# Kernel tuning notes

Measured on AMD Instinct MI355X. Metric: run time of the kernel, lower is better.

The kernel has to match this reference:

```python
import jax, jax.numpy as jnp
import numpy as np

T, NTOK, D = 8, 32768, 128
N_ENTIRE, COMP_LEN, COMP_DIM = 65536, 8, 64


def _layer_norm(v, w, b, eps=1e-5):
    m = v.mean(-1, keepdims=True)
    c = v - m
    var = (c * c).mean(-1, keepdims=True)
    return c * jax.lax.rsqrt(var + eps) * w + b


def setup_inputs() -> dict:
    key = jax.random.key(0)
    ks = jax.random.split(key, 8)
    x = jax.random.normal(ks[0], (T, NTOK, D), jnp.float32)
    padded_node_mask = jnp.ones((T, NTOK), dtype=bool)  # all tokens are nodes
    # unique per-timestamp scatter indices into the 'entire node' axis
    node_idx = jax.vmap(lambda k: jax.random.permutation(k, N_ENTIRE)[:NTOK])(
        jax.random.split(ks[1], T)).astype(jnp.int32)
    s = 0.02
    return dict(
        x=x,
        ln1_w=jnp.ones((D,), jnp.float32), ln1_b=jnp.zeros((D,), jnp.float32),
        w1=jax.random.normal(ks[2], (D, 2 * COMP_DIM), jnp.float32) * s,
        b1=jnp.zeros((2 * COMP_DIM,), jnp.float32),
        w2=jax.random.normal(ks[3], (2 * COMP_DIM, COMP_DIM), jnp.float32) * s,
        b2=jnp.zeros((COMP_DIM,), jnp.float32),
        lnf_w=jnp.ones((COMP_LEN * COMP_DIM,), jnp.float32),
        lnf_b=jnp.zeros((COMP_LEN * COMP_DIM,), jnp.float32),
        padded_node_mask=padded_node_mask,
        node_idx=node_idx,
        n_entire=N_ENTIRE,
    )


def reference(x, ln1_w, ln1_b, w1, b1, w2, b2, lnf_w, lnf_b,
              padded_node_mask, node_idx, n_entire):
    t, ntok, d = x.shape
    # encode_layer_norm over all tokens
    xn = _layer_norm(x, ln1_w, ln1_b)
    # nodes = xn[padded_node_mask].reshape(t, ntok, d); mask is all-True here
    nodes = jnp.where(padded_node_mask[..., None], xn, 0.0)
    # scga._to_entire: scatter nodes into [t, n_entire, d] (zeros elsewhere)
    tenodes = jnp.zeros((t, n_entire, d), x.dtype)
    tenodes = tenodes.at[jnp.arange(t)[:, None], node_idx].set(nodes)
    # eval mode: np.array_split(arange(n_entire), comp_len) = equal contiguous groups
    g = n_entire // COMP_LEN
    xg = tenodes.reshape(t, COMP_LEN, g, d)  # [t, L, g, d]
    # per-group MLP (Linear->GELU->(Dropout=id)->Linear) then mean over group
    h = jax.nn.gelu(jnp.einsum('tlgd,de->tlge', xg, w1) + b1, approximate=False)
    c = jnp.einsum('tlge,ec->tlgc', h, w2) + b2
    comp = c.mean(axis=2)  # [t, L, comp_dim]
    compressed = _layer_norm(comp.reshape(t, 1, COMP_LEN * COMP_DIM), lnf_w, lnf_b)
    # orthogonality loss over the L compressed components (exact torch pair loop)
    f = comp.transpose(1, 0, 2).reshape(COMP_LEN, -1)  # [L, t*comp_dim]
    fn = f / jnp.linalg.norm(f, axis=-1, keepdims=True)
    dots = []
    for i in range(COMP_LEN - 1):
        for j in range(1, COMP_LEN):
            dots.append(jnp.sum(fn[i] * fn[j]) / jnp.sum(fn[i] + fn[j]))
    ortho_loss = jnp.mean(jnp.stack(dots) ** 2)
    return compressed, ortho_loss
```

## Files before the change

### kernel.cpp

```cpp
#include <hip/hip_runtime.h>
#include <math.h>

#define TT 8
#define NTOK 32768
#define DD 128
#define LCOMP 8
#define GSZ 8192
#define CDIM 64
#define EDIM 128
#define NPART 32

#define TOKB 64
#define TILES 4
#define NBLK (TT*NTOK/(TOKB*TILES))

#define O_CZERO 0
#define O_W2BT  256
#define O_W1BT  (256 + EDIM*CDIM*2)
#define O_CSUMP (O_W1BT + DD*EDIM*2)

typedef __attribute__((ext_vector_type(8))) short bf16x8;
typedef __attribute__((ext_vector_type(4))) float f32x4;

__device__ __forceinline__ ushort f2bf(float f) {
    union { float f; uint u; } c; c.f = f;
    uint u = c.u;
    return (ushort)((u + 0x7FFFu + ((u >> 16) & 1u)) >> 16);
}

__device__ __forceinline__ float gelu_f(float a) {
    float x = a * 0.70710678118654752f;
    float ax = fabsf(x);
    float t = 1.0f / (1.0f + 0.3275911f * ax);
    float p = t * (0.254829592f + t * (-0.284496736f + t * (1.421413741f +
              t * (-1.453152027f + t * 1.061405429f))));
    float e = __expf(-x * x);
    float er = copysignf(1.0f - p * e, x);
    return 0.5f * a * (1.0f + er);
}

__global__ void prep_kernel(const float* __restrict__ w1, const float* __restrict__ b1,
                            const float* __restrict__ w2,
                            ushort* __restrict__ w1bt, ushort* __restrict__ w2bt,
                            float* __restrict__ czero, float* __restrict__ csum_p) {
    int gid = blockIdx.x * 256 + threadIdx.x;
    if (gid < DD * EDIM) {
        int j = gid >> 7, d = gid & 127;
        int slot = (d >> 3) ^ (j & 7);
        w1bt[j * 128 + slot * 8 + (d & 7)] = f2bf(w1[d * EDIM + j]);
    }
    if (gid < EDIM * CDIM) {
        int k = gid >> 7, jj = gid & 127;
        w2bt[k * 128 + jj] = f2bf(w2[jj * CDIM + k]);
    }
    if (gid < CDIM) {
        float a2 = 0.f;
        for (int dd = 0; dd < EDIM; ++dd)
            a2 += gelu_f(b1[dd]) * w2[dd * CDIM + gid];
        czero[gid] = a2;
    }
#pragma unroll
    for (int i = 0; i < 8; ++i)
        csum_p[gid + i * 16384] = 0.f;
}

__global__ __launch_bounds__(256, 2)
void main_kernel(const float* __restrict__ x,
                 const float* __restrict__ ln1w, const float* __restrict__ ln1b,
                 const float* __restrict__ b1g,
                 const ushort* __restrict__ w1bt, const ushort* __restrict__ w2bt,
                 const float* __restrict__ czero,
                 const int* __restrict__ node_idx,
                 float* __restrict__ csum_p) {
    __shared__ ushort s_xn[TOKB * DD];
    __shared__ ushort s_h[TOKB * DD];
    __shared__ float  s_acc[LCOMP * CDIM];

    const int tid = threadIdx.x;
    const int w   = tid >> 6;
    const int ln  = tid & 63;
    const int cs  = ln >> 4;
    const int row = w * 16 + (ln & 15);
    const int bid = blockIdx.x;
    const size_t base0 = (size_t)bid * (TOKB * TILES);

    s_acc[tid] = 0.f; s_acc[tid + 256] = 0.f;

    const float b1v0 = b1g[w * 32 + (ln & 15)];
    const float b1v1 = b1g[w * 32 + 16 + (ln & 15)];
    float czv[4];
#pragma unroll
    for (int kt = 0; kt < 4; ++kt) czv[kt] = czero[kt * 16 + (ln & 15)];

    float v[32];
    {
        const float* xp = x + (base0 + row) * DD + cs * 32;
#pragma unroll
        for (int sx = 0; sx < 8; ++sx) {
            float4 f = *(const float4*)(xp + sx * 4);
            v[sx*4+0]=f.x; v[sx*4+1]=f.y; v[sx*4+2]=f.z; v[sx*4+3]=f.w;
        }
    }

    for (int tile = 0; tile < TILES; ++tile) {
        {
            float s = 0.f, q = 0.f;
#pragma unroll
            for (int i2 = 0; i2 < 32; ++i2) { s += v[i2]; q += v[i2]*v[i2]; }
            s += __shfl_xor(s, 16, 64); q += __shfl_xor(q, 16, 64);
            s += __shfl_xor(s, 32, 64); q += __shfl_xor(q, 32, 64);
            float m   = s * (1.f/128.f);
            float var = q * (1.f/128.f) - m*m;
            float rs  = rsqrtf(var + 1e-5f);
#pragma unroll
            for (int sx = 0; sx < 8; ++sx) {
                float4 w4 = *(const float4*)(ln1w + cs*32 + sx*4);
                float4 b4 = *(const float4*)(ln1b + cs*32 + sx*4);
                v[sx*4+0] = (v[sx*4+0]-m)*rs*w4.x + b4.x;
                v[sx*4+1] = (v[sx*4+1]-m)*rs*w4.y + b4.y;
                v[sx*4+2] = (v[sx*4+2]-m)*rs*w4.z + b4.z;
                v[sx*4+3] = (v[sx*4+3]-m)*rs*w4.w + b4.w;
            }
        }
#pragma unroll
        for (int u = 0; u < 4; ++u) {
            uint4 pk;
            pk.x = f2bf(v[u*8+0]) | ((uint)f2bf(v[u*8+1]) << 16);
            pk.y = f2bf(v[u*8+2]) | ((uint)f2bf(v[u*8+3]) << 16);
            pk.z = f2bf(v[u*8+4]) | ((uint)f2bf(v[u*8+5]) << 16);
            pk.w = f2bf(v[u*8+6]) | ((uint)f2bf(v[u*8+7]) << 16);
            int slot = (cs * 4 + u) ^ (row & 7);
            *(uint4*)((char*)s_xn + row * 256 + slot * 16) = pk;
        }
        __syncthreads();

        if (tile + 1 < TILES) {
            const float* xp = x + (base0 + (tile + 1) * TOKB + row) * DD + cs * 32;
#pragma unroll
            for (int sx = 0; sx < 8; ++sx) {
                float4 f = *(const float4*)(xp + sx * 4);
                v[sx*4+0]=f.x; v[sx*4+1]=f.y; v[sx*4+2]=f.z; v[sx*4+3]=f.w;
            }
        }

        bf16x8 b1f[2][4];
#pragma unroll
        for (int jt = 0; jt < 2; ++jt)
#pragma unroll
            for (int ks = 0; ks < 4; ++ks) {
                int jrow = w * 32 + jt * 16 + (ln & 15);
                int slot = (ks * 4 + cs) ^ (jrow & 7);
                b1f[jt][ks] = *(const bf16x8*)((const char*)w1bt + jrow * 256 + slot * 16);
            }
#pragma unroll
        for (int tt = 0; tt < 4; ++tt) {
            bf16x8 a4[4];
            int ar = tt * 16 + (ln & 15);
#pragma unroll
            for (int ks = 0; ks < 4; ++ks) {
                int slot = (ks * 4 + cs) ^ (ar & 7);
                a4[ks] = *(const bf16x8*)((const char*)s_xn + ar * 256 + slot * 16);
            }
            f32x4 ac0 = {0.f,0.f,0.f,0.f}, ac1 = {0.f,0.f,0.f,0.f};
#pragma unroll
            for (int ks = 0; ks < 4; ++ks) {
                ac0 = __builtin_amdgcn_mfma_f32_16x16x32_bf16(a4[ks], b1f[0][ks], ac0, 0, 0, 0);
                ac1 = __builtin_amdgcn_mfma_f32_16x16x32_bf16(a4[ks], b1f[1][ks], ac1, 0, 0, 0);
            }
            int hrb = tt * 16 + cs * 4;
            int j0  = w * 32 + (ln & 15);
            int j1  = j0 + 16;
#pragma unroll
            for (int r = 0; r < 4; ++r) {
                float h0 = gelu_f(ac0[r] + b1v0);
                float h1 = gelu_f(ac1[r] + b1v1);
                int hrow = hrb + r;
                int sl0 = (j0 >> 3) ^ (hrow & 7);
                int sl1 = (j1 >> 3) ^ (hrow & 7);
                *(ushort*)((char*)s_h + hrow*256 + sl0*16 + (j0 & 7)*2) = f2bf(h0);
                *(ushort*)((char*)s_h + hrow*256 + sl1*16 + (j1 & 7)*2) = f2bf(h1);
            }
        }
        __syncthreads();

        {
            bf16x8 a4[4];
            int ar = w * 16 + (ln & 15);
#pragma unroll
            for (int ks = 0; ks < 4; ++ks) {
                int slot = (ks * 4 + cs) ^ (ar & 7);
                a4[ks] = *(const bf16x8*)((const char*)s_h + ar * 256 + slot * 16);
            }
            int tok0 = w * 16 + cs * 4;
            int4 li = *(const int4*)(node_idx + base0 + (size_t)tile * TOKB + tok0);
            int l0 = li.x >> 13, l1 = li.y >> 13, l2 = li.z >> 13, l3 = li.w >> 13;
#pragma unroll
            for (int kt = 0; kt < 4; ++kt) {
                bf16x8 bfr[4];
                int krow = kt * 16 + (ln & 15);
#pragma unroll
                for (int ks = 0; ks < 4; ++ks)
                    bfr[ks] = *(const bf16x8*)(w2bt + krow * EDIM + ks * 32 + cs * 8);
                f32x4 acc = {0.f,0.f,0.f,0.f};
#pragma unroll
                for (int ks = 0; ks < 4; ++ks)
                    acc = __builtin_amdgcn_mfma_f32_16x16x32_bf16(a4[ks], bfr[ks], acc, 0, 0, 0);
                int k = kt * 16 + (ln & 15);
                float czk = czv[kt];
                atomicAdd(&s_acc[l0 * CDIM + k], acc[0] - czk);
                atomicAdd(&s_acc[l1 * CDIM + k], acc[1] - czk);
                atomicAdd(&s_acc[l2 * CDIM + k], acc[2] - czk);
                atomicAdd(&s_acc[l3 * CDIM + k], acc[3] - czk);
            }
        }
        __syncthreads();
    }

    {
        int t8 = (bid >> 7) * LCOMP;
        int p  = bid & (NPART - 1);
#pragma unroll
        for (int i2 = 0; i2 < 2; ++i2) {
            int idx = tid + i2 * 256;
            int l = idx >> 6, k = idx & 63;
            atomicAdd(&csum_p[(p * 64 + t8 + l) * 64 + k], s_acc[idx]);
        }
    }
}

__global__ void fin_kernel(const float* __restrict__ csum_p, const float* __restrict__ czero,
                           const float* __restrict__ b2,
                           const float* __restrict__ lnfw, const float* __restrict__ lnfb,
                           float* __restrict__ out) {
    __shared__ float comp[TT * LCOMP * CDIM];
    __shared__ float norm_s[LCOMP], sum_s[LCOMP], red[8];
    int tid = threadIdx.x;

    for (int idx = tid; idx < TT * LCOMP * CDIM; idx += 512) {
        int bin = idx >> 6, k = idx & 63;
        float s = 0.f;
        for (int p = 0; p < NPART; ++p) s += csum_p[(p * 64 + bin) * 64 + k];
        comp[idx] = s * (1.f / GSZ) + czero[k] + b2[k];
    }
    __syncthreads();

    int wave = tid >> 6, lane = tid & 63;

    {
        int t = wave;
        float s = 0.f, q = 0.f;
        for (int e = lane; e < 512; e += 64) {
            float v = comp[t * 512 + e];
            s += v; q += v * v;
        }
#pragma unroll
        for (int off = 32; off > 0; off >>= 1) {
            s += __shfl_xor(s, off, 64);
            q += __shfl_xor(q, off, 64);
        }
        float m = s * (1.f / 512.f);
        float var = q * (1.f / 512.f) - m * m;
        float rs = rsqrtf(var + 1e-5f);
        for (int e = lane; e < 512; e += 64) {
            float v = comp[t * 512 + e];
            out[t * 512 + e] = (v - m) * rs * lnfw[e] + lnfb[e];
        }
    }

    {
        int l = wave;
        float s2 = 0.f, s1 = 0.f;
        for (int qd = lane; qd < 512; qd += 64) {
            int t = qd >> 6, k = qd & 63;
            float v = comp[t * 512 + l * 64 + k];
            s2 += v * v; s1 += v;
        }
#pragma unroll
        for (int off = 32; off > 0; off >>= 1) {
            s2 += __shfl_xor(s2, off, 64);
            s1 += __shfl_xor(s1, off, 64);
        }
        if (lane == 0) { norm_s[l] = sqrtf(s2); sum_s[l] = s1; }
    }
    __syncthreads();

    float loss_part = 0.f;
    for (int p = wave; p < 49; p += 8) {
        int i = p / 7, j = 1 + p % 7;
        float d = 0.f;
        for (int qd = lane; qd < 512; qd += 64) {
            int t = qd >> 6, k = qd & 63;
            d += comp[t * 512 + i * 64 + k] * comp[t * 512 + j * 64 + k];
        }
#pragma unroll
        for (int off = 32; off > 0; off >>= 1) d += __shfl_xor(d, off, 64);
        float ni = norm_s[i], nj = norm_s[j];
        float dot = (d / (ni * nj)) / (sum_s[i] / ni + sum_s[j] / nj);
        loss_part += dot * dot;
    }
    if (lane == 0) red[wave] = loss_part;
    __syncthreads();
    if (tid == 0) {
        float tot = 0.f;
        for (int w2_ = 0; w2_ < 8; ++w2_) tot += red[w2_];
        out[4096] = tot * (1.f / 49.f);
    }
}

extern "C" void kernel_launch(void* const* d_in, const int* in_sizes, int n_in,
                              void* d_out, int out_size, void* d_ws, size_t ws_size,
                              hipStream_t stream) {
    const float* x    = (const float*)d_in[0];
    const float* ln1w = (const float*)d_in[1];
    const float* ln1b = (const float*)d_in[2];
    const float* w1   = (const float*)d_in[3];
    const float* b1   = (const float*)d_in[4];
    const float* w2   = (const float*)d_in[5];
    const float* b2   = (const float*)d_in[6];
    const float* lnfw = (const float*)d_in[7];
    const float* lnfb = (const float*)d_in[8];
    const int* node_idx = (const int*)d_in[10];
    float* out = (float*)d_out;

    char* wsb = (char*)d_ws;
    float*  czero  = (float*)(wsb + O_CZERO);
    ushort* w2bt   = (ushort*)(wsb + O_W2BT);
    ushort* w1bt   = (ushort*)(wsb + O_W1BT);
    float*  csum_p = (float*)(wsb + O_CSUMP);

    prep_kernel<<<64, 256, 0, stream>>>(w1, b1, w2, w1bt, w2bt, czero, csum_p);
    main_kernel<<<NBLK, 256, 0, stream>>>(x, ln1w, ln1b, b1, w1bt, w2bt, czero,
                                          node_idx, csum_p);
    fin_kernel<<<1, 512, 0, stream>>>(csum_p, czero, b2, lnfw, lnfb, out);
}
```

Baseline: 365.0 us.

## Keep MLP weights in registers and run per-wave token batches without block syncs

Each wave now loads all W1 and W2 bf16 fragments into registers once and handles its own 16-token batches. LayerNorm output goes straight into MFMA operand registers, and the GELU result makes only a short round trip through per-wave shared memory. Block-level __syncthreads between tiles and shared staging of xn are gone, and the transposed formulation lets bias and czero seed the accumulators. Blocks are larger and there are fewer global partial sums. The cost is much higher register pressure, which may reduce occupancy, plus per-token shared atomics with possible bank contention.

After: 391.0 us. 7.1% more time.

```diff
diff --git a/kernel.cpp b/kernel.cpp
--- a/kernel.cpp
+++ b/kernel.cpp
@@ -8,11 +8,13 @@
 #define GSZ 8192
 #define CDIM 64
 #define EDIM 128
-#define NPART 32
-
-#define TOKB 64
-#define TILES 4
-#define NBLK (TT*NTOK/(TOKB*TILES))
+#define NPART 8
+
+#define BATCH 16
+#define BPW 8
+#define WAVES 4
+#define TOKBLK (WAVES*BPW*BATCH)
+#define NBLK (TT*NTOK/TOKBLK)
 
 #define O_CZERO 0
 #define O_W2BT  256
@@ -46,8 +48,7 @@
     int gid = blockIdx.x * 256 + threadIdx.x;
     if (gid < DD * EDIM) {
         int j = gid >> 7, d = gid & 127;
-        int slot = (d >> 3) ^ (j & 7);
-        w1bt[j * 128 + slot * 8 + (d & 7)] = f2bf(w1[d * EDIM + j]);
+        w1bt[j * 128 + d] = f2bf(w1[d * EDIM + j]);
     }
     if (gid < EDIM * CDIM) {
         int k = gid >> 7, jj = gid & 127;
@@ -60,7 +61,7 @@
         czero[gid] = a2;
     }
 #pragma unroll
-    for (int i = 0; i < 8; ++i)
+    for (int i = 0; i < 2; ++i)
         csum_p[gid + i * 16384] = 0.f;
 }
 
@@ -72,158 +73,153 @@
                  const float* __restrict__ czero,
                  const int* __restrict__ node_idx,
                  float* __restrict__ csum_p) {
-    __shared__ ushort s_xn[TOKB * DD];
-    __shared__ ushort s_h[TOKB * DD];
-    __shared__ float  s_acc[LCOMP * CDIM];
+    __shared__ ushort s_h[WAVES * 2048];
+    __shared__ float  s_acc[LCOMP * 65];
 
     const int tid = threadIdx.x;
     const int w   = tid >> 6;
     const int ln  = tid & 63;
     const int cs  = ln >> 4;
-    const int row = w * 16 + (ln & 15);
+    const int tk  = ln & 15;
     const int bid = blockIdx.x;
-    const size_t base0 = (size_t)bid * (TOKB * TILES);
-
-    s_acc[tid] = 0.f; s_acc[tid + 256] = 0.f;
-
-    const float b1v0 = b1g[w * 32 + (ln & 15)];
-    const float b1v1 = b1g[w * 32 + 16 + (ln & 15)];
-    float czv[4];
-#pragma unroll
-    for (int kt = 0; kt < 4; ++kt) czv[kt] = czero[kt * 16 + (ln & 15)];
+
+    for (int idx = tid; idx < LCOMP * 65; idx += 256) s_acc[idx] = 0.f;
+
+    bf16x8 w1f[8][4];
+#pragma unroll
+    for (int jt = 0; jt < 8; ++jt)
+#pragma unroll
+        for (int ks = 0; ks < 4; ++ks)
+            w1f[jt][ks] = *(const bf16x8*)(w1bt + (jt*16 + tk)*128 + ks*32 + cs*8);
+    bf16x8 w2f[4][4];
+#pragma unroll
+    for (int kt = 0; kt < 4; ++kt)
+#pragma unroll
+        for (int ks = 0; ks < 4; ++ks)
+            w2f[kt][ks] = *(const bf16x8*)(w2bt + (kt*16 + tk)*128 + ks*32 + cs*8);
+    f32x4 b1v[8];
+#pragma unroll
+    for (int jt = 0; jt < 8; ++jt)
+        b1v[jt] = *(const f32x4*)(b1g + jt*16 + cs*4);
+    f32x4 czv[4];
+#pragma unroll
+    for (int kt = 0; kt < 4; ++kt)
+        czv[kt] = -*(const f32x4*)(czero + kt*16 + cs*4);
+
+    __syncthreads();
+
+    const size_t wbase = (size_t)bid * TOKBLK + w * (BPW * BATCH);
+    char* hbase = (char*)s_h + w * 4096;
 
     float v[32];
     {
-        const float* xp = x + (base0 + row) * DD + cs * 32;
-#pragma unroll
-        for (int sx = 0; sx < 8; ++sx) {
-            float4 f = *(const float4*)(xp + sx * 4);
-            v[sx*4+0]=f.x; v[sx*4+1]=f.y; v[sx*4+2]=f.z; v[sx*4+3]=f.w;
-        }
-    }
-
-    for (int tile = 0; tile < TILES; ++tile) {
-        {
-            float s = 0.f, q = 0.f;
-#pragma unroll
-            for (int i2 = 0; i2 < 32; ++i2) { s += v[i2]; q += v[i2]*v[i2]; }
-            s += __shfl_xor(s, 16, 64); q += __shfl_xor(q, 16, 64);
-            s += __shfl_xor(s, 32, 64); q += __shfl_xor(q, 32, 64);
-            float m   = s * (1.f/128.f);
-            float var = q * (1.f/128.f) - m*m;
-            float rs  = rsqrtf(var + 1e-5f);
-#pragma unroll
-            for (int sx = 0; sx < 8; ++sx) {
-                float4 w4 = *(const float4*)(ln1w + cs*32 + sx*4);
-                float4 b4 = *(const float4*)(ln1b + cs*32 + sx*4);
-                v[sx*4+0] = (v[sx*4+0]-m)*rs*w4.x + b4.x;
-                v[sx*4+1] = (v[sx*4+1]-m)*rs*w4.y + b4.y;
-                v[sx*4+2] = (v[sx*4+2]-m)*rs*w4.z + b4.z;
-                v[sx*4+3] = (v[sx*4+3]-m)*rs*w4.w + b4.w;
+        const float* xp = x + (wbase + tk) * (size_t)DD;
+#pragma unroll
+        for (int m = 0; m < 4; ++m) {
+            *(float4*)(v + m*8)     = *(const float4*)(xp + m*32 + cs*8);
+            *(float4*)(v + m*8 + 4) = *(const float4*)(xp + m*32 + cs*8 + 4);
+        }
+    }
+
+    for (int b = 0; b < BPW; ++b) {
+        const size_t tb = wbase + (size_t)b * BATCH;
+        const int lg = node_idx[tb + tk] >> 13;
+
+        float s = 0.f, q = 0.f;
+#pragma unroll
+        for (int i = 0; i < 32; ++i) { s += v[i]; q += v[i]*v[i]; }
+        s += __shfl_xor(s, 16, 64); q += __shfl_xor(q, 16, 64);
+        s += __shfl_xor(s, 32, 64); q += __shfl_xor(q, 32, 64);
+        float mean = s * (1.f/128.f);
+        float var  = q * (1.f/128.f) - mean*mean;
+        float rs   = rsqrtf(var + 1e-5f);
+
+        bf16x8 xnf[4];
+#pragma unroll
+        for (int m = 0; m < 4; ++m) {
+            const float* lwp = ln1w + m*32 + cs*8;
+            const float* lbp = ln1b + m*32 + cs*8;
+            float4 lw0 = *(const float4*)(lwp),   lw1 = *(const float4*)(lwp + 4);
+            float4 lb0 = *(const float4*)(lbp),   lb1 = *(const float4*)(lbp + 4);
+            float g0 = (v[m*8+0]-mean)*rs*lw0.x + lb0.x;
+            float g1 = (v[m*8+1]-mean)*rs*lw0.y + lb0.y;
+            float g2 = (v[m*8+2]-mean)*rs*lw0.z + lb0.z;
+            float g3 = (v[m*8+3]-mean)*rs*lw0.w + lb0.w;
+            float g4 = (v[m*8+4]-mean)*rs*lw1.x + lb1.x;
+            float g5 = (v[m*8+5]-mean)*rs*lw1.y + lb1.y;
+            float g6 = (v[m*8+6]-mean)*rs*lw1.z + lb1.z;
+            float g7 = (v[m*8+7]-mean)*rs*lw1.w + lb1.w;
+            uint4 pk;
+            pk.x = f2bf(g0) | ((uint)f2bf(g1) << 16);
+            pk.y = f2bf(g2) | ((uint)f2bf(g3) << 16);
+            pk.z = f2bf(g4) | ((uint)f2bf(g5) << 16);
+            pk.w = f2bf(g6) | ((uint)f2bf(g7) << 16);
+            xnf[m] = __builtin_bit_cast(bf16x8, pk);
+        }
+
+        if (b + 1 < BPW) {
+            const float* xq = x + (tb + BATCH + tk) * (size_t)DD;
+#pragma unroll
+            for (int m = 0; m < 4; ++m) {
+                *(float4*)(v + m*8)     = *(const float4*)(xq + m*32 + cs*8);
+                *(float4*)(v + m*8 + 4) = *(const float4*)(xq + m*32 + cs*8 + 4);
             }
         }
-#pragma unroll
-        for (int u = 0; u < 4; ++u) {
-            uint4 pk;
-            pk.x = f2bf(v[u*8+0]) | ((uint)f2bf(v[u*8+1]) << 16);
-            pk.y = f2bf(v[u*8+2]) | ((uint)f2bf(v[u*8+3]) << 16);
-            pk.z = f2bf(v[u*8+4]) | ((uint)f2bf(v[u*8+5]) << 16);
-            pk.w = f2bf(v[u*8+6]) | ((uint)f2bf(v[u*8+7]) << 16);
-            int slot = (cs * 4 + u) ^ (row & 7);
-            *(uint4*)((char*)s_xn + row * 256 + slot * 16) = pk;
-        }
-        __syncthreads();
-
-        if (tile + 1 < TILES) {
-            const float* xp = x + (base0 + (tile + 1) * TOKB + row) * DD + cs * 32;
-#pragma unroll
-            for (int sx = 0; sx < 8; ++sx) {
-                float4 f = *(const float4*)(xp + sx * 4);
-                v[sx*4+0]=f.x; v[sx*4+1]=f.y; v[sx*4+2]=f.z; v[sx*4+3]=f.w;
-            }
-        }
-
-        bf16x8 b1f[2][4];
-#pragma unroll
-        for (int jt = 0; jt < 2; ++jt)
-#pragma unroll
-            for (int ks = 0; ks < 4; ++ks) {
-                int jrow = w * 32 + jt * 16 + (ln & 15);
-                int slot = (ks * 4 + cs) ^ (jrow & 7);
-                b1f[jt][ks] = *(const bf16x8*)((const char*)w1bt + jrow * 256 + slot * 16);
-            }
-#pragma unroll
-        for (int tt = 0; tt < 4; ++tt) {
-            bf16x8 a4[4];
-            int ar = tt * 16 + (ln & 15);
-#pragma unroll
-            for (int ks = 0; ks < 4; ++ks) {
-                int slot = (ks * 4 + cs) ^ (ar & 7);
-                a4[ks] = *(const bf16x8*)((const char*)s_xn + ar * 256 + slot * 16);
-            }
-            f32x4 ac0 = {0.f,0.f,0.f,0.f}, ac1 = {0.f,0.f,0.f,0.f};
-#pragma unroll
-            for (int ks = 0; ks < 4; ++ks) {
-                ac0 = __builtin_amdgcn_mfma_f32_16x16x32_bf16(a4[ks], b1f[0][ks], ac0, 0, 0, 0);
-                ac1 = __builtin_amdgcn_mfma_f32_16x16x32_bf16(a4[ks], b1f[1][ks], ac1, 0, 0, 0);
-            }
-            int hrb = tt * 16 + cs * 4;
-            int j0  = w * 32 + (ln & 15);
-            int j1  = j0 + 16;
-#pragma unroll
-            for (int r = 0; r < 4; ++r) {
-                float h0 = gelu_f(ac0[r] + b1v0);
-                float h1 = gelu_f(ac1[r] + b1v1);
-                int hrow = hrb + r;
-                int sl0 = (j0 >> 3) ^ (hrow & 7);
-                int sl1 = (j1 >> 3) ^ (hrow & 7);
-                *(ushort*)((char*)s_h + hrow*256 + sl0*16 + (j0 & 7)*2) = f2bf(h0);
-                *(ushort*)((char*)s_h + hrow*256 + sl1*16 + (j1 & 7)*2) = f2bf(h1);
-            }
-        }
-        __syncthreads();
-
-        {
-            bf16x8 a4[4];
-            int ar = w * 16 + (ln & 15);
-#pragma unroll
-            for (int ks = 0; ks < 4; ++ks) {
-                int slot = (ks * 4 + cs) ^ (ar & 7);
-                a4[ks] = *(const bf16x8*)((const char*)s_h + ar * 256 + slot * 16);
-            }
-            int tok0 = w * 16 + cs * 4;
-            int4 li = *(const int4*)(node_idx + base0 + (size_t)tile * TOKB + tok0);
-            int l0 = li.x >> 13, l1 = li.y >> 13, l2 = li.z >> 13, l3 = li.w >> 13;
-#pragma unroll
-            for (int kt = 0; kt < 4; ++kt) {
-                bf16x8 bfr[4];
-                int krow = kt * 16 + (ln & 15);
-#pragma unroll
-                for (int ks = 0; ks < 4; ++ks)
-                    bfr[ks] = *(const bf16x8*)(w2bt + krow * EDIM + ks * 32 + cs * 8);
-                f32x4 acc = {0.f,0.f,0.f,0.f};
-#pragma unroll
-                for (int ks = 0; ks < 4; ++ks)
-                    acc = __builtin_amdgcn_mfma_f32_16x16x32_bf16(a4[ks], bfr[ks], acc, 0, 0, 0);
-                int k = kt * 16 + (ln & 15);
-                float czk = czv[kt];
-                atomicAdd(&s_acc[l0 * CDIM + k], acc[0] - czk);
-                atomicAdd(&s_acc[l1 * CDIM + k], acc[1] - czk);
-                atomicAdd(&s_acc[l2 * CDIM + k], acc[2] - czk);
-                atomicAdd(&s_acc[l3 * CDIM + k], acc[3] - czk);
-            }
-        }
-        __syncthreads();
-    }
+
+        f32x4 acc1[8];
+#pragma unroll
+        for (int jt = 0; jt < 8; ++jt) acc1[jt] = b1v[jt];
+#pragma unroll
+        for (int ks = 0; ks < 4; ++ks)
+#pragma unroll
+            for (int jt = 0; jt < 8; ++jt)
+                acc1[jt] = __builtin_amdgcn_mfma_f32_16x16x32_bf16(
+                    w1f[jt][ks], xnf[ks], acc1[jt], 0, 0, 0);
+
+#pragma unroll
+        for (int jt = 0; jt < 8; ++jt) {
+            float g0 = gelu_f(acc1[jt][0]);
+            float g1 = gelu_f(acc1[jt][1]);
+            float g2 = gelu_f(acc1[jt][2]);
+            float g3 = gelu_f(acc1[jt][3]);
+            uint2 pk2;
+            pk2.x = f2bf(g0) | ((uint)f2bf(g1) << 16);
+            pk2.y = f2bf(g2) | ((uint)f2bf(g3) << 16);
+            int c16 = (jt*2 + (cs >> 1)) ^ tk;
+            *(uint2*)(hbase + tk*256 + c16*16 + (cs & 1)*8) = pk2;
+        }
+        bf16x8 B2[4];
+#pragma unroll
+        for (int ks = 0; ks < 4; ++ks) {
+            int c16 = (ks*4 + cs) ^ tk;
+            B2[ks] = *(const bf16x8*)(hbase + tk*256 + c16*16);
+        }
+
+        f32x4 acc2[4];
+#pragma unroll
+        for (int kt = 0; kt < 4; ++kt) acc2[kt] = czv[kt];
+#pragma unroll
+        for (int ks = 0; ks < 4; ++ks)
+#pragma unroll
+            for (int kt = 0; kt < 4; ++kt)
+                acc2[kt] = __builtin_amdgcn_mfma_f32_16x16x32_bf16(
+                    w2f[kt][ks], B2[ks], acc2[kt], 0, 0, 0);
+
+#pragma unroll
+        for (int kt = 0; kt < 4; ++kt)
+#pragma unroll
+            for (int r = 0; r < 4; ++r)
+                atomicAdd(&s_acc[lg*65 + kt*16 + cs*4 + r], acc2[kt][r]);
+    }
+
+    __syncthreads();
 
     {
-        int t8 = (bid >> 7) * LCOMP;
+        int t8 = (bid >> 6) * LCOMP;
         int p  = bid & (NPART - 1);
-#pragma unroll
-        for (int i2 = 0; i2 < 2; ++i2) {
-            int idx = tid + i2 * 256;
+        for (int idx = tid; idx < LCOMP * CDIM; idx += 256) {
             int l = idx >> 6, k = idx & 63;
-            atomicAdd(&csum_p[(p * 64 + t8 + l) * 64 + k], s_acc[idx]);
+            atomicAdd(&csum_p[(p * 64 + t8 + l) * 64 + k], s_acc[l*65 + k]);
         }
     }
 }
```
